# Kernel tuning notes

Hardware: AMD Instinct MI355X
Metric: run time of the kernel (lower is better)

## Reference

```python
import jax, jax.numpy as jnp
import numpy as np

D_KEY = 512
D_VALUE = 512
D_MEM_HIDDEN = 64
BATCH = 65536


def setup_inputs() -> dict:
    key = jax.random.key(0)
    ks = jax.random.split(key, 6)
    return {
        "key": jax.random.normal(ks[0], (BATCH, D_KEY), dtype=jnp.float32),
        "value": jax.random.normal(ks[1], (BATCH, D_VALUE), dtype=jnp.float32),
        # memory MLP weights (the stored memory)
        "mem_W1": jax.random.normal(ks[2], (D_MEM_HIDDEN, D_KEY), dtype=jnp.float32) * 0.02,
        "mem_b1": jnp.zeros((D_MEM_HIDDEN,), dtype=jnp.float32),
        "mem_W2": jax.random.normal(ks[3], (D_VALUE, D_MEM_HIDDEN), dtype=jnp.float32) * 0.02,
        "mem_b2": jnp.zeros((D_VALUE,), dtype=jnp.float32),
        # per-dimension precision head
        "prec_W": jax.random.normal(ks[4], (D_VALUE, D_KEY), dtype=jnp.float32) * 0.01,
        "prec_b": jnp.ones((D_VALUE,), dtype=jnp.float32),
    }


def reference(key, value, mem_W1, mem_b1, mem_W2, mem_b2, prec_W, prec_b):
    """Faithful translation of MemoryModule.free_energy.

    F = prec * clamp(value - pred, -3, 3)^2 - log(prec), averaged over d_value.
    """
    # predict: two-layer MLP with exact (erf) GELU, matching torch F.gelu default
    h = jax.nn.gelu(key @ mem_W1.T + mem_b1, approximate=False)  # (B, H)
    pred = h @ mem_W2.T + mem_b2                                  # (B, Dv)
    # precision head: softplus + 0.01, always positive
    prec = jax.nn.softplus(key @ prec_W.T + prec_b) + 0.01        # (B, Dv)
    error = jnp.clip(value - pred, -3.0, 3.0)                     # (B, Dv)
    F_per_dim = prec * error * error - jnp.log(prec)
    F_scalar = F_per_dim.mean(axis=-1)                            # (B,)
    return (F_scalar, pred, prec, error)
```

## Files before the change

kernel.cpp:

```cpp
#include <hip/hip_runtime.h>
#include <hip/hip_bf16.h>

#define BATCH 65536
#define DK 512
#define DV 512
#define DH 64
#define BM 64
#define NT (DV / 16)

typedef __attribute__((ext_vector_type(8))) short bf16x8;
typedef __attribute__((ext_vector_type(4))) float f32x4;

__device__ short g_wb[327680];

__device__ __forceinline__ short f2bf(float f) {
    union { __hip_bfloat16 h; short s; } u;
    u.h = __float2bfloat16(f);
    return u.s;
}

__global__ __launch_bounds__(256) void conv_weights(
    const float* __restrict__ W1, const float* __restrict__ W2,
    const float* __restrict__ Wp)
{
    int i = blockIdx.x * 256 + threadIdx.x;
    long off = (long)i * 4;
    const float* src;
    if (off < 32768)       src = W1 + off;
    else if (off < 65536)  src = W2 + (off - 32768);
    else                   src = Wp + (off - 65536);
    float4 v = *reinterpret_cast<const float4*>(src);
    short4 s;
    s.x = f2bf(v.x); s.y = f2bf(v.y); s.z = f2bf(v.z); s.w = f2bf(v.w);
    *reinterpret_cast<short4*>(g_wb + off) = s;
}

struct StReg { bf16x8 v[4]; };

__device__ __forceinline__ StReg stage_load(const short* __restrict__ src, int tid) {
    StReg s;
    #pragma unroll
    for (int ld = 0; ld < 4; ++ld)
        s.v[ld] = *reinterpret_cast<const bf16x8*>(
            reinterpret_cast<const char*>(src) + ld * 4096 + tid * 16);
    return s;
}

__device__ __forceinline__ void stage_write(char* buf, const StReg& s, int tid) {
    #pragma unroll
    for (int ld = 0; ld < 4; ++ld) {
        int o = ld * 4096 + tid * 16;
        int w = o ^ (((o >> 10) & 7) << 4);
        *reinterpret_cast<bf16x8*>(buf + w) = s.v[ld];
    }
}

#define WPA 0
#define WPB 16384
#define W2A 32768
#define W2B (32768 + 2048)
#define HOF 36864

__global__ __launch_bounds__(256, 3) void fused_free_energy(
    const float* __restrict__ key, const float* __restrict__ value,
    const float* __restrict__ b1, const float* __restrict__ b2,
    const float* __restrict__ pb,
    float* __restrict__ outF, float* __restrict__ outPred,
    float* __restrict__ outPrec, float* __restrict__ outErr)
{
    __shared__ __align__(16) char lds[45056];

    const short* W1b = g_wb;
    const short* W2b = g_wb + 32768;
    const short* Wpb = g_wb + 65536;

    const int tid  = threadIdx.x;
    const int wave = tid >> 6;
    const int lane = tid & 63;
    const int lh   = lane & 15;
    const int lg   = lane >> 4;
    const long row0 = (long)blockIdx.x * BM;

    bf16x8 kreg[16];
    #pragma unroll
    for (int c = 0; c < 2; ++c) {
        const float4* kin = reinterpret_cast<const float4*>(key + (row0 + c * 32) * DK);
        #pragma unroll
        for (int i = 0; i < 16; ++i) {
            int idx = i * 256 + tid;
            int r = idx >> 7, c4 = idx & 127;
            float4 v = kin[idx];
            short4 s;
            s.x = f2bf(v.x); s.y = f2bf(v.y); s.z = f2bf(v.z); s.w = f2bf(v.w);
            int byte = (r * 1024 + c4 * 8) ^ ((r & 7) << 4);
            *reinterpret_cast<short4*>(lds + byte) = s;
        }
        __syncthreads();
        if ((wave >> 1) == c) {
            int rr = (wave & 1) * 16 + lh;
            #pragma unroll
            for (int kk = 0; kk < 16; ++kk) {
                int byte = (rr * 1024 + kk * 64 + lg * 16) ^ ((rr & 7) << 4);
                kreg[kk] = *reinterpret_cast<const bf16x8*>(lds + byte);
            }
        }
        __syncthreads();
    }

    const f32x4 zf = {0.f, 0.f, 0.f, 0.f};

    {
        StReg st = stage_load(W1b, tid);
        stage_write(lds + WPA, st, tid);
        __syncthreads();
        #pragma unroll
        for (int jt = 0; jt < 4; ++jt) {
            char* cbuf = lds + ((jt & 1) ? WPB : WPA);
            StReg nx;
            if (jt < 3) nx = stage_load(W1b + (jt + 1) * 16 * DK, tid);
            f32x4 acc = zf;
            #pragma unroll
            for (int kk = 0; kk < 16; ++kk) {
                int byte = (lh * 1024 + kk * 64 + lg * 16) ^ ((lh & 7) << 4);
                bf16x8 af = *reinterpret_cast<const bf16x8*>(cbuf + byte);
                acc = __builtin_amdgcn_mfma_f32_16x16x32_bf16(af, kreg[kk], acc, 0, 0, 0);
            }
            float4 b1v = *reinterpret_cast<const float4*>(b1 + jt * 16 + lg * 4);
            float b1a[4] = {b1v.x, b1v.y, b1v.z, b1v.w};
            short hs[4];
            #pragma unroll
            for (int r = 0; r < 4; ++r) {
                float z = acc[r] + b1a[r];
                float g = 0.5f * z * (1.0f + erff(z * 0.70710678f));
                hs[r] = f2bf(g);
            }
            int hb = HOF + wave * 2048 + ((lh * 128 + jt * 32 + lg * 8) ^ ((lh & 7) << 4));
            short4 hv = {hs[0], hs[1], hs[2], hs[3]};
            *reinterpret_cast<short4*>(lds + hb) = hv;
            if (jt < 3) stage_write(lds + ((jt & 1) ? WPA : WPB), nx, tid);
            __syncthreads();
        }
    }

    bf16x8 hreg[2];
    #pragma unroll
    for (int kh = 0; kh < 2; ++kh) {
        int byte = (lh * 128 + kh * 64 + lg * 16) ^ ((lh & 7) << 4);
        hreg[kh] = *reinterpret_cast<const bf16x8*>(lds + HOF + wave * 2048 + byte);
    }

    {
        StReg st = stage_load(Wpb, tid);
        const bool w2a = (tid < 128);
        bf16x8 w2r;
        if (w2a) w2r = *reinterpret_cast<const bf16x8*>(
                     reinterpret_cast<const char*>(W2b) + tid * 16);
        stage_write(lds + WPA, st, tid);
        if (w2a) {
            int o = tid * 16;
            *reinterpret_cast<bf16x8*>(lds + W2A + (o ^ (((o >> 7) & 7) << 4))) = w2r;
        }
        __syncthreads();

        float facc = 0.f;
        const long grow = row0 + wave * 16 + lh;

        for (int it = 0; it < NT; ++it) {
            char* wpc = lds + ((it & 1) ? WPB : WPA);
            char* w2c = lds + ((it & 1) ? W2B : W2A);

            StReg nx; bf16x8 w2n;
            if (it + 1 < NT) {
                nx = stage_load(Wpb + (it + 1) * 16 * DK, tid);
                if (w2a) w2n = *reinterpret_cast<const bf16x8*>(
                             reinterpret_cast<const char*>(W2b) + (it + 1) * 2048 + tid * 16);
            }

            f32x4 acc3 = zf;
            #pragma unroll
            for (int kk = 0; kk < 16; ++kk) {
                int byte = (lh * 1024 + kk * 64 + lg * 16) ^ ((lh & 7) << 4);
                bf16x8 af = *reinterpret_cast<const bf16x8*>(wpc + byte);
                acc3 = __builtin_amdgcn_mfma_f32_16x16x32_bf16(af, kreg[kk], acc3, 0, 0, 0);
            }
            f32x4 acc2 = zf;
            #pragma unroll
            for (int kh = 0; kh < 2; ++kh) {
                int byte = (lh * 128 + kh * 64 + lg * 16) ^ ((lh & 7) << 4);
                bf16x8 af = *reinterpret_cast<const bf16x8*>(w2c + byte);
                acc2 = __builtin_amdgcn_mfma_f32_16x16x32_bf16(af, hreg[kh], acc2, 0, 0, 0);
            }

            int nb = it * 16 + lg * 4;
            float4 b2v = *reinterpret_cast<const float4*>(b2 + nb);
            float4 pbv = *reinterpret_cast<const float4*>(pb + nb);
            float b2a[4] = {b2v.x, b2v.y, b2v.z, b2v.w};
            float pba[4] = {pbv.x, pbv.y, pbv.z, pbv.w};
            long ga = grow * DV + nb;
            float4 val = *reinterpret_cast<const float4*>(value + ga);
            float va[4] = {val.x, val.y, val.z, val.w};
            float prv[4], pcv[4], erv[4];
            #pragma unroll
            for (int r = 0; r < 4; ++r) {
                float pred = acc2[r] + b2a[r];
                float z    = acc3[r] + pba[r];
                float prec = fmaxf(z, 0.f) + log1pf(expf(-fabsf(z))) + 0.01f;
                float err  = fminf(fmaxf(va[r] - pred, -3.f), 3.f);
                prv[r] = pred; pcv[r] = prec; erv[r] = err;
                facc += prec * err * err - logf(prec);
            }
            float4 pr4 = {prv[0], prv[1], prv[2], prv[3]};
            float4 pc4 = {pcv[0], pcv[1], pcv[2], pcv[3]};
            float4 er4 = {erv[0], erv[1], erv[2], erv[3]};
            *reinterpret_cast<float4*>(outPred + ga) = pr4;
            *reinterpret_cast<float4*>(outPrec + ga) = pc4;
            *reinterpret_cast<float4*>(outErr  + ga) = er4;

            if (it + 1 < NT) {
                stage_write(lds + ((it & 1) ? WPA : WPB), nx, tid);
                if (w2a) {
                    int o = tid * 16;
                    *reinterpret_cast<bf16x8*>(
                        lds + ((it & 1) ? W2A : W2B) + (o ^ (((o >> 7) & 7) << 4))) = w2n;
                }
            }
            __syncthreads();
        }

        facc += __shfl_xor(facc, 16, 64);
        facc += __shfl_xor(facc, 32, 64);
        if (lane < 16) outF[grow] = facc * (1.0f / 512.0f);
    }
}

extern "C" void kernel_launch(void* const* d_in, const int* in_sizes, int n_in,
                              void* d_out, int out_size, void* d_ws, size_t ws_size,
                              hipStream_t stream) {
    const float* key   = (const float*)d_in[0];
    const float* value = (const float*)d_in[1];
    const float* W1    = (const float*)d_in[2];
    const float* b1    = (const float*)d_in[3];
    const float* W2    = (const float*)d_in[4];
    const float* b2    = (const float*)d_in[5];
    const float* Wp    = (const float*)d_in[6];
    const float* pb    = (const float*)d_in[7];

    float* outF    = (float*)d_out;
    float* outPred = outF + BATCH;
    float* outPrec = outPred + (long)BATCH * DV;
    float* outErr  = outPrec + (long)BATCH * DV;

    conv_weights<<<320, 256, 0, stream>>>(W1, W2, Wp);
    fused_free_energy<<<BATCH / BM, 256, 0, stream>>>(key, value, b1, b2, pb,
                                                      outF, outPred, outPrec, outErr);
}
```

Measured before the change: 300.1 us.

## Reuse weight LDS buffer for hidden activations, raise occupancy, use fast math intrinsics

Removes the dedicated hidden-activation LDS region by holding GELU outputs in registers until the W1 loop ends, then writing them into the freed weight buffer. This cuts LDS from 44KB to 36KB so launch bounds can target 4 blocks per CU instead of 3. It also swaps log1pf/expf/logf for the fast __logf/__expf intrinsics, and batches output stores in pairs of iterations. In exchange it adds extra syncs, more live registers, and slightly lower softplus accuracy.

New measurement: 413.2 us, median of 4. +37.7%, slower.

```diff
diff --git a/kernel.cpp b/kernel.cpp
--- a/kernel.cpp
+++ b/kernel.cpp
@@ -59,16 +59,15 @@
 #define WPB 16384
 #define W2A 32768
 #define W2B (32768 + 2048)
-#define HOF 36864
-
-__global__ __launch_bounds__(256, 3) void fused_free_energy(
+
+__global__ __launch_bounds__(256, 4) void fused_free_energy(
     const float* __restrict__ key, const float* __restrict__ value,
     const float* __restrict__ b1, const float* __restrict__ b2,
     const float* __restrict__ pb,
     float* __restrict__ outF, float* __restrict__ outPred,
     float* __restrict__ outPrec, float* __restrict__ outErr)
 {
-    __shared__ __align__(16) char lds[45056];
+    __shared__ __align__(16) char lds[36864];
 
     const short* W1b = g_wb;
     const short* W2b = g_wb + 32768;
@@ -109,6 +108,7 @@
 
     const f32x4 zf = {0.f, 0.f, 0.f, 0.f};
 
+    short hs_all[16];
     {
         StReg st = stage_load(W1b, tid);
         stage_write(lds + WPA, st, tid);
@@ -127,27 +127,32 @@
             }
             float4 b1v = *reinterpret_cast<const float4*>(b1 + jt * 16 + lg * 4);
             float b1a[4] = {b1v.x, b1v.y, b1v.z, b1v.w};
-            short hs[4];
             #pragma unroll
             for (int r = 0; r < 4; ++r) {
                 float z = acc[r] + b1a[r];
                 float g = 0.5f * z * (1.0f + erff(z * 0.70710678f));
-                hs[r] = f2bf(g);
-            }
-            int hb = HOF + wave * 2048 + ((lh * 128 + jt * 32 + lg * 8) ^ ((lh & 7) << 4));
-            short4 hv = {hs[0], hs[1], hs[2], hs[3]};
-            *reinterpret_cast<short4*>(lds + hb) = hv;
+                hs_all[jt * 4 + r] = f2bf(g);
+            }
             if (jt < 3) stage_write(lds + ((jt & 1) ? WPA : WPB), nx, tid);
             __syncthreads();
         }
+        #pragma unroll
+        for (int jt = 0; jt < 4; ++jt) {
+            int hb = WPA + wave * 2048 + ((lh * 128 + jt * 32 + lg * 8) ^ ((lh & 7) << 4));
+            short4 hv = {hs_all[jt * 4 + 0], hs_all[jt * 4 + 1],
+                         hs_all[jt * 4 + 2], hs_all[jt * 4 + 3]};
+            *reinterpret_cast<short4*>(lds + hb) = hv;
+        }
+        __syncthreads();
     }
 
     bf16x8 hreg[2];
     #pragma unroll
     for (int kh = 0; kh < 2; ++kh) {
         int byte = (lh * 128 + kh * 64 + lg * 16) ^ ((lh & 7) << 4);
-        hreg[kh] = *reinterpret_cast<const bf16x8*>(lds + HOF + wave * 2048 + byte);
-    }
+        hreg[kh] = *reinterpret_cast<const bf16x8*>(lds + WPA + wave * 2048 + byte);
+    }
+    __syncthreads();
 
     {
         StReg st = stage_load(Wpb, tid);
@@ -164,6 +169,8 @@
 
         float facc = 0.f;
         const long grow = row0 + wave * 16 + lh;
+        float4 sv_pr, sv_pc, sv_er;
+        long sv_ga = 0;
 
         for (int it = 0; it < NT; ++it) {
             char* wpc = lds + ((it & 1) ? WPB : WPA);
@@ -204,17 +211,24 @@
             for (int r = 0; r < 4; ++r) {
                 float pred = acc2[r] + b2a[r];
                 float z    = acc3[r] + pba[r];
-                float prec = fmaxf(z, 0.f) + log1pf(expf(-fabsf(z))) + 0.01f;
+                float prec = fmaxf(z, 0.f) + __logf(1.0f + __expf(-fabsf(z))) + 0.01f;
                 float err  = fminf(fmaxf(va[r] - pred, -3.f), 3.f);
                 prv[r] = pred; pcv[r] = prec; erv[r] = err;
-                facc += prec * err * err - logf(prec);
+                facc += prec * err * err - __logf(prec);
             }
             float4 pr4 = {prv[0], prv[1], prv[2], prv[3]};
             float4 pc4 = {pcv[0], pcv[1], pcv[2], pcv[3]};
             float4 er4 = {erv[0], erv[1], erv[2], erv[3]};
-            *reinterpret_cast<float4*>(outPred + ga) = pr4;
-            *reinterpret_cast<float4*>(outPrec + ga) = pc4;
-            *reinterpret_cast<float4*>(outErr  + ga) = er4;
+            if ((it & 1) == 0) {
+                sv_pr = pr4; sv_pc = pc4; sv_er = er4; sv_ga = ga;
+            } else {
+                *reinterpret_cast<float4*>(outPred + sv_ga) = sv_pr;
+                *reinterpret_cast<float4*>(outPred + ga)    = pr4;
+                *reinterpret_cast<float4*>(outPrec + sv_ga) = sv_pc;
+                *reinterpret_cast<float4*>(outPrec + ga)    = pc4;
+                *reinterpret_cast<float4*>(outErr  + sv_ga) = sv_er;
+                *reinterpret_cast<float4*>(outErr  + ga)    = er4;
+            }
 
             if (it + 1 < NT) {
                 stage_write(lds + ((it & 1) ? WPA : WPB), nx, tid);
```
